# Kernel tuning notes

Hardware: AMD Instinct MI355X
Metric: run time of the kernel (lower is better)

## Reference

```python
import jax, jax.numpy as jnp
import numpy as np

PATCH_SIZE = 128
IMG = 256


def _circle_perimeter(r_o, c_o, radius):
    # skimage.draw.circle_perimeter, method='bresenham' (midpoint circle),
    # including the duplicate octant-boundary points that skimage emits.
    rr, cc = [], []
    c, r = 0, radius
    d = 3 - 2 * radius
    while c <= r:
        rr += [r, -r, r, -r, c, -c, c, -c]
        cc += [c, c, -c, -c, r, r, -r, -r]
        if d < 0:
            d += 4 * c + 6
        else:
            d += 4 * (c - r) + 10
            r -= 1
        c += 1
    return np.asarray(rr) + r_o, np.asarray(cc) + c_o


def _radial_indices(patch_size, img):
    cy, cx = img // 2, img // 2
    rr_all, cc_all, seg_all = [], [], []
    for radius in range(1, patch_size - 1):  # radii 1..patch_size-2
        rr, cc = _circle_perimeter(cy, cx, radius)
        rr_all.append(rr)
        cc_all.append(cc)
        seg_all.append(np.full(rr.shape[0], radius - 1))
    return (np.concatenate(rr_all).astype(np.int32),
            np.concatenate(cc_all).astype(np.int32),
            np.concatenate(seg_all).astype(np.int32))


def setup_inputs() -> dict:
    key = jax.random.key(0)
    k1, k2 = jax.random.split(key)
    inp = jax.random.normal(k1, (64, 3, IMG, IMG), dtype=jnp.float32)
    tgt = jax.random.normal(k2, (64, 3, IMG, IMG), dtype=jnp.float32)
    w = np.float32(np.arange(0, 1, 1 / (PATCH_SIZE - 1)))  # length 127
    weights = jnp.asarray(w / np.sum(w))
    rr_idx, cc_idx, seg_ids = _radial_indices(PATCH_SIZE, IMG)
    return {"input": inp, "target": tgt, "weights": weights,
            "rr_idx": jnp.asarray(rr_idx), "cc_idx": jnp.asarray(cc_idx),
            "seg_ids": jnp.asarray(seg_ids)}


def reference(input, target, weights, rr_idx, cc_idx, seg_ids):
    B, C = input.shape[0], input.shape[1]
    R = weights.shape[0]          # patch_size - 1 curve bins
    nseg = R - 1                  # radii 1..patch_size-2
    f1 = jnp.fft.fft2(input)      # complex64 [B,C,H,W]
    f2 = jnp.fft.fft2(target)
    p1 = f1[:, :, rr_idx, cc_idx]  # [B,C,Ntot]
    p2 = f2[:, :, rr_idx, cc_idx]
    # original sums num/den over ALL dims (batch+channel+perimeter points)
    cross = jnp.sum(p1 * jnp.conj(p2), axis=(0, 1))        # [Ntot] complex
    pw1 = jnp.sum(jnp.abs(p1) ** 2, axis=(0, 1))           # [Ntot]
    pw2 = jnp.sum(jnp.abs(p2) ** 2, axis=(0, 1))
    num = jnp.abs(jax.ops.segment_sum(cross, seg_ids, num_segments=nseg))
    den = (jax.ops.segment_sum(pw1, seg_ids, num_segments=nseg) *
           jax.ops.segment_sum(pw2, seg_ids, num_segments=nseg))
    curve = jnp.concatenate([jnp.ones((1,), jnp.float32),
                             (num / jnp.sqrt(den)).astype(jnp.float32)])  # [R]
    # curve is identical across (b, c); Linear(R,1,bias=False) then total sum
    curve_full = jnp.broadcast_to(curve, (B, C, R))
    return jnp.sum(curve_full @ weights)
```

## Files before the change

kernel.cpp:

```cpp
#include <hip/hip_runtime.h>
#include <math.h>

#define NSEG 126

__device__ __forceinline__ unsigned bitrev8(unsigned v) { return __brev(v) >> 24; }

template <int K>
__device__ __forceinline__ void fftK(float2 x[][4], int lane) {
    const float PI = 3.14159265358979323846f;
    {
        float s, c;
        __sincosf(-PI * (float)lane * (1.0f / 128.0f), &s, &c);
        #pragma unroll
        for (int k = 0; k < K; k++) {
            float2 u, t, d;
            u = x[k][0]; t = x[k][2];
            x[k][0] = make_float2(u.x + t.x, u.y + t.y);
            d = make_float2(u.x - t.x, u.y - t.y);
            x[k][2] = make_float2(d.x * c - d.y * s, d.x * s + d.y * c);
            u = x[k][1]; t = x[k][3];
            x[k][1] = make_float2(u.x + t.x, u.y + t.y);
            d = make_float2(u.x - t.x, u.y - t.y);
            x[k][3] = make_float2(d.x * s + d.y * c, -d.x * c + d.y * s);
        }
    }
    {
        float s, c;
        __sincosf(-PI * (float)lane * (1.0f / 64.0f), &s, &c);
        #pragma unroll
        for (int k = 0; k < K; k++) {
            float2 u, t, d;
            u = x[k][0]; t = x[k][1];
            x[k][0] = make_float2(u.x + t.x, u.y + t.y);
            d = make_float2(u.x - t.x, u.y - t.y);
            x[k][1] = make_float2(d.x * c - d.y * s, d.x * s + d.y * c);
            u = x[k][2]; t = x[k][3];
            x[k][2] = make_float2(u.x + t.x, u.y + t.y);
            d = make_float2(u.x - t.x, u.y - t.y);
            x[k][3] = make_float2(d.x * c - d.y * s, d.x * s + d.y * c);
        }
    }
    #pragma unroll
    for (int hbit = 5; hbit >= 0; hbit--) {
        int h = 1 << hbit;
        int j = lane & (h - 1);
        float s, c;
        __sincosf(-PI * (float)j / (float)h, &s, &c);
        bool up = (lane & h) != 0;
        #pragma unroll
        for (int k = 0; k < K; k++) {
            #pragma unroll
            for (int i = 0; i < 4; i++) {
                float px = __shfl_xor(x[k][i].x, h);
                float py = __shfl_xor(x[k][i].y, h);
                if (up) {
                    float dx = px - x[k][i].x, dy = py - x[k][i].y;
                    x[k][i] = make_float2(dx * c - dy * s, dx * s + dy * c);
                } else {
                    x[k][i] = make_float2(x[k][i].x + px, x[k][i].y + py);
                }
            }
        }
    }
}

__global__ void prep_zero(float* acc, int* counts) {
    int i = threadIdx.x;
    if (i < NSEG * 3) acc[i] = 0.f;
    if (i < 128) counts[i] = 0;
}

__device__ __forceinline__ bool keep_point(int r, int c) {
    return (c > 128) || (c == 128 && r > 128);
}

__global__ void prep_hist(const int* __restrict__ rr, const int* __restrict__ cc,
                          int n, int* counts) {
    int i = blockIdx.x * 256 + threadIdx.x;
    if (i < n) {
        int c = cc[i], r = rr[i];
        if (keep_point(r, c)) atomicAdd(&counts[255 - c], 1);
    }
}

__global__ void prep_scan(const int* __restrict__ counts, int* starts, int* cursor) {
    int lane = threadIdx.x;
    int2 c = reinterpret_cast<const int2*>(counts)[lane];
    int lsum = c.x + c.y;
    int pre = lsum;
    #pragma unroll
    for (int off = 1; off < 64; off <<= 1) {
        int v = __shfl_up(pre, off);
        if (lane >= off) pre += v;
    }
    int excl = pre - lsum;
    int2 outv = make_int2(excl, excl + c.x);
    reinterpret_cast<int2*>(starts)[lane] = outv;
    reinterpret_cast<int2*>(cursor)[lane] = outv;
    if (lane == 63) starts[128] = excl + c.x + c.y;
}

__global__ void prep_scatter(const int* __restrict__ rr, const int* __restrict__ cc,
                             const int* __restrict__ seg, int n, int* cursor,
                             int* b_pack) {
    int i = blockIdx.x * 256 + threadIdx.x;
    if (i < n) {
        int c = cc[i], r = rr[i];
        if (keep_point(r, c)) {
            int j = 255 - c;
            int pos = atomicAdd(&cursor[j], 1);
            int pr = (int)bitrev8((unsigned)r);
            int pm = (int)bitrev8((unsigned)(256 - r) & 255);
            b_pack[pos] = pr | (pm << 8) | (seg[i] << 16);
        }
    }
}

__global__ __launch_bounds__(512) void rowfft_kernel(
    const float* __restrict__ inp, const float* __restrict__ tgt,
    float2* __restrict__ G, int pair_base)
{
    __shared__ float2 T[256 * 17];
    int bid    = blockIdx.x;
    int plocal = bid >> 4;
    int rowgrp = bid & 15;
    int wv     = threadIdx.x >> 6;
    int lane   = threadIdx.x & 63;
    size_t base = (((size_t)(pair_base + plocal)) << 16)
                + ((size_t)((rowgrp << 4) + (wv << 1)) << 8);
    const float* s1 = inp + base;
    const float* s2 = tgt + base;

    float2 x[2][4];
    #pragma unroll
    for (int k = 0; k < 2; k++)
        #pragma unroll
        for (int i = 0; i < 4; i++) {
            int e = (k << 8) + i * 64 + lane;
            x[k][i] = make_float2(s1[e], s2[e]);
        }
    fftK<2>(x, lane);

    #pragma unroll
    for (int k = 0; k < 2; k++)
        #pragma unroll
        for (int i = 0; i < 4; i++)
            T[(i * 64 + lane) * 17 + (wv << 1) + k] = x[k][i];
    __syncthreads();

    float2* dst = G + (((size_t)plocal) << 16) + (rowgrp << 4);
    int xl = threadIdx.x & 15;
    int qb = threadIdx.x >> 4;
    #pragma unroll
    for (int ii = 0; ii < 8; ii++) {
        int q = qb + (ii << 5);
        dst[q * 256 + xl] = T[q * 17 + xl];
    }
}

__global__ __launch_bounds__(256) void colfft_gather_kernel(
    const float2* __restrict__ G, const int* __restrict__ starts,
    const int* __restrict__ b_pack, float* __restrict__ acc)
{
    __shared__ float2 Fb[4][2][256];
    __shared__ float accl[NSEG * 3];
    int tid    = threadIdx.x;
    int wv     = tid >> 6;
    int lane   = tid & 63;
    int plocal = blockIdx.x >> 4;
    int b      = blockIdx.x & 15;
    int jbase  = (b << 3) + (wv << 1);

    for (int i = tid; i < NSEG * 3; i += 256) accl[i] = 0.f;
    __syncthreads();

    const float2* Gp = G + (((size_t)plocal) << 16);
    int cols[4];
    cols[0] = jbase + 1;   cols[1] = 255 - jbase;
    cols[2] = jbase + 2;   cols[3] = 254 - jbase;

    float2 x[4][4];
    #pragma unroll
    for (int k = 0; k < 4; k++) {
        int q = (int)bitrev8((unsigned)cols[k]);
        const float2* col = Gp + ((size_t)q << 8);
        #pragma unroll
        for (int i = 0; i < 4; i++) x[k][i] = col[i * 64 + lane];
    }

    fftK<4>(x, lane);

    float2* F_lo = &Fb[wv][0][0];
    float2* F_hi = &Fb[wv][1][0];
    #pragma unroll
    for (int kb = 0; kb < 2; kb++) {
        #pragma unroll
        for (int i = 0; i < 4; i++) {
            F_lo[i * 64 + lane] = x[2 * kb + 0][i];
            F_hi[i * 64 + lane] = x[2 * kb + 1][i];
        }
        int j = jbase + kb;
        int s0 = starts[j], s1 = starts[j + 1];
        int e  = s0 + lane;
        int pk = (e < s1) ? b_pack[e] : 0;
        while (e < s1) {
            int e2  = e + 64;
            int pk2 = (e2 < s1) ? b_pack[e2] : 0;
            float2 a = F_hi[pk & 255];
            float2 m = F_lo[(pk >> 8) & 255];
            int sg = pk >> 16;
            float f1x = a.x + m.x, f1y = a.y - m.y;
            float dx  = a.x - m.x, dy  = a.y + m.y;
            atomicAdd(&accl[sg * 3 + 0], f1x * dy - f1y * dx);
            atomicAdd(&accl[sg * 3 + 1], f1x * f1x + f1y * f1y);
            atomicAdd(&accl[sg * 3 + 2], dx * dx + dy * dy);
            e = e2; pk = pk2;
        }
    }
    __syncthreads();

    for (int i = tid; i < NSEG * 3; i += 256) {
        float v = accl[i];
        if (v != 0.f) atomicAdd(&acc[i], v);
    }
}

__global__ void final_kernel(const float* __restrict__ acc, const float* __restrict__ w,
                             float* __restrict__ out, float scale) {
    int lane = threadIdx.x;
    float val = 0.f;
    for (int s = lane; s < NSEG; s += 64) {
        float cr = acc[s * 3 + 0];
        float p1 = acc[s * 3 + 1];
        float p2 = acc[s * 3 + 2];
        float den = p1 * p2;
        float curve = den > 0.f ? fabsf(cr) * rsqrtf(den) : 0.f;
        val += curve * w[s + 1];
    }
    if (lane == 0) val += w[0];
    #pragma unroll
    for (int off = 32; off > 0; off >>= 1) val += __shfl_down(val, off);
    if (lane == 0) out[0] = scale * val;
}

extern "C" void kernel_launch(void* const* d_in, const int* in_sizes, int n_in,
                              void* d_out, int out_size, void* d_ws, size_t ws_size,
                              hipStream_t stream)
{
    const float* inp = (const float*)d_in[0];
    const float* tgt = (const float*)d_in[1];
    const float* wts = (const float*)d_in[2];
    const int*   rr  = (const int*)d_in[3];
    const int*   cc  = (const int*)d_in[4];
    const int*   sg  = (const int*)d_in[5];
    int npts   = in_sizes[3];
    int npairs = in_sizes[0] >> 16;

    char* ws = (char*)d_ws;
    float* acc    = (float*)(ws + 0);
    int*   counts = (int*)(ws + 2048);
    int*   starts = (int*)(ws + 2560);
    int*   cursor = (int*)(ws + 3584);
    int*   b_pack = (int*)(ws + 4096);
    size_t goff = 4096 + (size_t)npts * 4;
    goff = (goff + 255) & ~(size_t)255;
    float2* G = (float2*)(ws + goff);

    size_t per_pair = (size_t)256 * 256 * sizeof(float2);
    int maxchunk = (int)((ws_size > goff ? (ws_size - goff) : 0) / per_pair);
    if (maxchunk < 1) maxchunk = 1;
    if (maxchunk > npairs) maxchunk = npairs;

    prep_zero<<<1, 512, 0, stream>>>(acc, counts);
    prep_hist<<<(npts + 255) / 256, 256, 0, stream>>>(rr, cc, npts, counts);
    prep_scan<<<1, 64, 0, stream>>>(counts, starts, cursor);
    prep_scatter<<<(npts + 255) / 256, 256, 0, stream>>>(rr, cc, sg, npts, cursor, b_pack);

    for (int pb = 0; pb < npairs; pb += maxchunk) {
        int cp = npairs - pb < maxchunk ? npairs - pb : maxchunk;
        rowfft_kernel<<<cp * 16, 512, 0, stream>>>(inp, tgt, G, pb);
        colfft_gather_kernel<<<cp * 16, 256, 0, stream>>>(G, starts, b_pack, acc);
    }

    final_kernel<<<1, 64, 0, stream>>>(acc, wts, (float*)d_out, (float)npairs);
}
```

Before: 267.5 us.

## Replace shuffle-based radix-2 FFT with register radix-16x16 FFT through LDS

```diff
diff --git a/kernel.cpp b/kernel.cpp
--- a/kernel.cpp
+++ b/kernel.cpp
@@ -2,66 +2,66 @@
 #include <math.h>
 
 #define NSEG 126
-
-__device__ __forceinline__ unsigned bitrev8(unsigned v) { return __brev(v) >> 24; }
-
-template <int K>
-__device__ __forceinline__ void fftK(float2 x[][4], int lane) {
-    const float PI = 3.14159265358979323846f;
-    {
+#define PI_F 3.14159265358979323846f
+#define C8 0.92387953251128675613f
+#define S8 0.38268343236508977173f
+#define R2C 0.70710678118654752440f
+
+__device__ __forceinline__ float2 cadd(float2 a, float2 b){ return make_float2(a.x+b.x, a.y+b.y); }
+__device__ __forceinline__ float2 csub(float2 a, float2 b){ return make_float2(a.x-b.x, a.y-b.y); }
+__device__ __forceinline__ float2 cmulf(float2 a, float c, float s){
+    return make_float2(fmaf(-a.y, s, a.x*c), fmaf(a.x, s, a.y*c));
+}
+__device__ __forceinline__ float2 mulmi(float2 a){ return make_float2(a.y, -a.x); }
+
+__device__ __forceinline__ void fft16(float2 a[16]) {
+    float2 u, d;
+    u=a[0]; d=csub(a[0],a[8]);  a[0]=cadd(u,a[8]);   a[8]=d;
+    u=a[1]; d=csub(a[1],a[9]);  a[1]=cadd(u,a[9]);   a[9]=cmulf(d,  C8, -S8);
+    u=a[2]; d=csub(a[2],a[10]); a[2]=cadd(u,a[10]);  a[10]=cmulf(d, R2C, -R2C);
+    u=a[3]; d=csub(a[3],a[11]); a[3]=cadd(u,a[11]);  a[11]=cmulf(d,  S8, -C8);
+    u=a[4]; d=csub(a[4],a[12]); a[4]=cadd(u,a[12]);  a[12]=mulmi(d);
+    u=a[5]; d=csub(a[5],a[13]); a[5]=cadd(u,a[13]);  a[13]=cmulf(d, -S8, -C8);
+    u=a[6]; d=csub(a[6],a[14]); a[6]=cadd(u,a[14]);  a[14]=cmulf(d, -R2C, -R2C);
+    u=a[7]; d=csub(a[7],a[15]); a[7]=cadd(u,a[15]);  a[15]=cmulf(d, -C8, -S8);
+    #pragma unroll
+    for (int h = 0; h < 16; h += 8) {
+        u=a[h+0]; d=csub(a[h+0],a[h+4]); a[h+0]=cadd(u,a[h+4]); a[h+4]=d;
+        u=a[h+1]; d=csub(a[h+1],a[h+5]); a[h+1]=cadd(u,a[h+5]); a[h+5]=cmulf(d, R2C, -R2C);
+        u=a[h+2]; d=csub(a[h+2],a[h+6]); a[h+2]=cadd(u,a[h+6]); a[h+6]=mulmi(d);
+        u=a[h+3]; d=csub(a[h+3],a[h+7]); a[h+3]=cadd(u,a[h+7]); a[h+7]=cmulf(d, -R2C, -R2C);
+    }
+    #pragma unroll
+    for (int q = 0; q < 16; q += 4) {
+        u=a[q+0]; d=csub(a[q+0],a[q+2]); a[q+0]=cadd(u,a[q+2]); a[q+2]=d;
+        u=a[q+1]; d=csub(a[q+1],a[q+3]); a[q+1]=cadd(u,a[q+3]); a[q+3]=mulmi(d);
+    }
+    #pragma unroll
+    for (int p = 0; p < 16; p += 2) {
+        u=a[p]; a[p]=cadd(u,a[p+1]); a[p+1]=csub(u,a[p+1]);
+    }
+}
+
+__device__ __constant__ int BR4[16] = {0,8,4,12,2,10,6,14,1,9,5,13,3,11,7,15};
+
+__device__ __forceinline__ void fft256_core(float2 x[16], float2* gb, int r) {
+    fft16(x);
+    #pragma unroll
+    for (int m = 1; m < 16; m++) {
         float s, c;
-        __sincosf(-PI * (float)lane * (1.0f / 128.0f), &s, &c);
-        #pragma unroll
-        for (int k = 0; k < K; k++) {
-            float2 u, t, d;
-            u = x[k][0]; t = x[k][2];
-            x[k][0] = make_float2(u.x + t.x, u.y + t.y);
-            d = make_float2(u.x - t.x, u.y - t.y);
-            x[k][2] = make_float2(d.x * c - d.y * s, d.x * s + d.y * c);
-            u = x[k][1]; t = x[k][3];
-            x[k][1] = make_float2(u.x + t.x, u.y + t.y);
-            d = make_float2(u.x - t.x, u.y - t.y);
-            x[k][3] = make_float2(d.x * s + d.y * c, -d.x * c + d.y * s);
-        }
-    }
-    {
-        float s, c;
-        __sincosf(-PI * (float)lane * (1.0f / 64.0f), &s, &c);
-        #pragma unroll
-        for (int k = 0; k < K; k++) {
-            float2 u, t, d;
-            u = x[k][0]; t = x[k][1];
-            x[k][0] = make_float2(u.x + t.x, u.y + t.y);
-            d = make_float2(u.x - t.x, u.y - t.y);
-            x[k][1] = make_float2(d.x * c - d.y * s, d.x * s + d.y * c);
-            u = x[k][2]; t = x[k][3];
-            x[k][2] = make_float2(u.x + t.x, u.y + t.y);
-            d = make_float2(u.x - t.x, u.y - t.y);
-            x[k][3] = make_float2(d.x * c - d.y * s, d.x * s + d.y * c);
-        }
-    }
-    #pragma unroll
-    for (int hbit = 5; hbit >= 0; hbit--) {
-        int h = 1 << hbit;
-        int j = lane & (h - 1);
-        float s, c;
-        __sincosf(-PI * (float)j / (float)h, &s, &c);
-        bool up = (lane & h) != 0;
-        #pragma unroll
-        for (int k = 0; k < K; k++) {
-            #pragma unroll
-            for (int i = 0; i < 4; i++) {
-                float px = __shfl_xor(x[k][i].x, h);
-                float py = __shfl_xor(x[k][i].y, h);
-                if (up) {
-                    float dx = px - x[k][i].x, dy = py - x[k][i].y;
-                    x[k][i] = make_float2(dx * c - dy * s, dx * s + dy * c);
-                } else {
-                    x[k][i] = make_float2(x[k][i].x + px, x[k][i].y + py);
-                }
-            }
-        }
-    }
+        __sincosf(-(PI_F / 128.0f) * (float)(r * BR4[m]), &s, &c);
+        x[m] = cmulf(x[m], c, s);
+    }
+    #pragma unroll
+    for (int m = 0; m < 16; m++)
+        gb[BR4[m] * 16 + ((r + BR4[m]) & 15)] = x[m];
+    float2 z[16];
+    #pragma unroll
+    for (int n1 = 0; n1 < 16; n1++)
+        z[n1] = gb[r * 16 + ((n1 + r) & 15)];
+    fft16(z);
+    #pragma unroll
+    for (int m = 0; m < 16; m++) x[m] = z[m];
 }
 
 __global__ void prep_zero(float* acc, int* counts) {
@@ -109,97 +109,107 @@
         if (keep_point(r, c)) {
             int j = 255 - c;
             int pos = atomicAdd(&cursor[j], 1);
-            int pr = (int)bitrev8((unsigned)r);
-            int pm = (int)bitrev8((unsigned)(256 - r) & 255);
-            b_pack[pos] = pr | (pm << 8) | (seg[i] << 16);
+            b_pack[pos] = r | (((256 - r) & 255) << 8) | (seg[i] << 16);
         }
     }
 }
 
-__global__ __launch_bounds__(512) void rowfft_kernel(
+__global__ __launch_bounds__(128, 4) void rowfft_kernel(
     const float* __restrict__ inp, const float* __restrict__ tgt,
     float2* __restrict__ G, int pair_base)
 {
-    __shared__ float2 T[256 * 17];
+    __shared__ float2 lds[256 * 9];
+    int tid    = threadIdx.x;
+    int wv     = tid >> 6;
+    int lane   = tid & 63;
+    int g      = lane >> 4;
+    int r      = lane & 15;
     int bid    = blockIdx.x;
-    int plocal = bid >> 4;
-    int rowgrp = bid & 15;
-    int wv     = threadIdx.x >> 6;
-    int lane   = threadIdx.x & 63;
-    size_t base = (((size_t)(pair_base + plocal)) << 16)
-                + ((size_t)((rowgrp << 4) + (wv << 1)) << 8);
-    const float* s1 = inp + base;
-    const float* s2 = tgt + base;
-
-    float2 x[2][4];
-    #pragma unroll
-    for (int k = 0; k < 2; k++)
-        #pragma unroll
-        for (int i = 0; i < 4; i++) {
-            int e = (k << 8) + i * 64 + lane;
-            x[k][i] = make_float2(s1[e], s2[e]);
-        }
-    fftK<2>(x, lane);
-
-    #pragma unroll
-    for (int k = 0; k < 2; k++)
-        #pragma unroll
-        for (int i = 0; i < 4; i++)
-            T[(i * 64 + lane) * 17 + (wv << 1) + k] = x[k][i];
-    __syncthreads();
-
-    float2* dst = G + (((size_t)plocal) << 16) + (rowgrp << 4);
-    int xl = threadIdx.x & 15;
-    int qb = threadIdx.x >> 4;
-    #pragma unroll
-    for (int ii = 0; ii < 8; ii++) {
-        int q = qb + (ii << 5);
-        dst[q * 256 + xl] = T[q * 17 + xl];
-    }
-}
-
-__global__ __launch_bounds__(256) void colfft_gather_kernel(
+    int plocal = bid >> 5;
+    int rowgrp = bid & 31;
+    int row    = (rowgrp << 3) + (wv << 2) + g;
+    size_t base = (((size_t)(pair_base + plocal)) << 16) + ((size_t)row << 8) + (r << 4);
+    const float4* s1 = (const float4*)(inp + base);
+    const float4* s2 = (const float4*)(tgt + base);
+
+    float4 A[4], B[4];
+    #pragma unroll
+    for (int i = 0; i < 4; i++) { A[i] = s1[i]; B[i] = s2[i]; }
+    float2 x[16];
+    #pragma unroll
+    for (int i = 0; i < 4; i++) {
+        x[4*i+0] = make_float2(A[i].x, B[i].x);
+        x[4*i+1] = make_float2(A[i].y, B[i].y);
+        x[4*i+2] = make_float2(A[i].z, B[i].z);
+        x[4*i+3] = make_float2(A[i].w, B[i].w);
+    }
+    float2* gb = lds + wv * 1040 + g * 260;
+    #pragma unroll
+    for (int n1 = 0; n1 < 16; n1++)
+        gb[n1 * 16 + ((r + n1) & 15)] = x[n1];
+    float2 y[16];
+    #pragma unroll
+    for (int n2 = 0; n2 < 16; n2++)
+        y[n2] = gb[r * 16 + ((n2 + r) & 15)];
+
+    fft256_core(y, gb, r);
+
+    __syncthreads();
+    int lrow = (wv << 2) + g;
+    #pragma unroll
+    for (int m = 0; m < 16; m++)
+        lds[(r + 16 * BR4[m]) * 9 + lrow] = y[m];
+    __syncthreads();
+
+    float2* dst = G + (((size_t)plocal) << 16) + (rowgrp << 3);
+    int xl = tid & 7;
+    int q8 = tid >> 3;
+    #pragma unroll
+    for (int ii = 0; ii < 16; ii++) {
+        int q = q8 + (ii << 4);
+        dst[q * 256 + xl] = lds[q * 9 + xl];
+    }
+}
+
+__global__ __launch_bounds__(128, 4) void colfft_gather_kernel(
     const float2* __restrict__ G, const int* __restrict__ starts,
     const int* __restrict__ b_pack, float* __restrict__ acc)
 {
-    __shared__ float2 Fb[4][2][256];
+    __shared__ float2 wbufs[2 * 1040];
     __shared__ float accl[NSEG * 3];
     int tid    = threadIdx.x;
     int wv     = tid >> 6;
     int lane   = tid & 63;
-    int plocal = blockIdx.x >> 4;
-    int b      = blockIdx.x & 15;
-    int jbase  = (b << 3) + (wv << 1);
-
-    for (int i = tid; i < NSEG * 3; i += 256) accl[i] = 0.f;
-    __syncthreads();
-
-    const float2* Gp = G + (((size_t)plocal) << 16);
-    int cols[4];
-    cols[0] = jbase + 1;   cols[1] = 255 - jbase;
-    cols[2] = jbase + 2;   cols[3] = 254 - jbase;
-
-    float2 x[4][4];
-    #pragma unroll
-    for (int k = 0; k < 4; k++) {
-        int q = (int)bitrev8((unsigned)cols[k]);
-        const float2* col = Gp + ((size_t)q << 8);
-        #pragma unroll
-        for (int i = 0; i < 4; i++) x[k][i] = col[i * 64 + lane];
-    }
-
-    fftK<4>(x, lane);
-
-    float2* F_lo = &Fb[wv][0][0];
-    float2* F_hi = &Fb[wv][1][0];
+    int g      = lane >> 4;
+    int r      = lane & 15;
+    int plocal = blockIdx.x >> 5;
+    int b      = blockIdx.x & 31;
+    int jbase  = (b << 2) + (wv << 1);
+
+    for (int i = tid; i < NSEG * 3; i += 128) accl[i] = 0.f;
+    __syncthreads();
+
+    int c = (g == 0) ? (jbase + 1) : (g == 1) ? (255 - jbase)
+          : (g == 2) ? (jbase + 2) : (254 - jbase);
+    const float2* col = G + (((size_t)plocal) << 16) + ((size_t)c << 8) + r;
+
+    float2 x[16];
+    #pragma unroll
+    for (int n2 = 0; n2 < 16; n2++) x[n2] = col[n2 << 4];
+
+    float2* gb = wbufs + wv * 1040 + g * 260;
+    fft256_core(x, gb, r);
+
+    #pragma unroll
+    for (int m = 0; m < 16; m++)
+        gb[r + 16 * BR4[m]] = x[m];
+
+    float2* wbuf = wbufs + wv * 1040;
     #pragma unroll
     for (int kb = 0; kb < 2; kb++) {
-        #pragma unroll
-        for (int i = 0; i < 4; i++) {
-            F_lo[i * 64 + lane] = x[2 * kb + 0][i];
-            F_hi[i * 64 + lane] = x[2 * kb + 1][i];
-        }
         int j = jbase + kb;
+        const float2* F_lo = wbuf + (2 * kb) * 260;
+        const float2* F_hi = wbuf + (2 * kb + 1) * 260;
         int s0 = starts[j], s1 = starts[j + 1];
         int e  = s0 + lane;
         int pk = (e < s1) ? b_pack[e] : 0;
@@ -219,7 +229,7 @@
     }
     __syncthreads();
 
-    for (int i = tid; i < NSEG * 3; i += 256) {
+    for (int i = tid; i < NSEG * 3; i += 128) {
         float v = accl[i];
         if (v != 0.f) atomicAdd(&acc[i], v);
     }
@@ -278,8 +288,8 @@
 
     for (int pb = 0; pb < npairs; pb += maxchunk) {
         int cp = npairs - pb < maxchunk ? npairs - pb : maxchunk;
-        rowfft_kernel<<<cp * 16, 512, 0, stream>>>(inp, tgt, G, pb);
-        colfft_gather_kernel<<<cp * 16, 256, 0, stream>>>(G, starts, b_pack, acc);
+        rowfft_kernel<<<cp * 32, 128, 0, stream>>>(inp, tgt, G, pb);
+        colfft_gather_kernel<<<cp * 32, 128, 0, stream>>>(G, starts, b_pack, acc);
     }
 
     final_kernel<<<1, 64, 0, stream>>>(acc, wts, (float*)d_out, (float)npairs);
```

Result: slower. 312.7 us (+16.9%).

## Store row FFT output row-major and transpose via shared tile in column pass

Applied to the files above, without the earlier changes.

```diff
diff --git a/kernel.cpp b/kernel.cpp
--- a/kernel.cpp
+++ b/kernel.cpp
@@ -64,10 +64,9 @@
     }
 }
 
-__global__ void prep_zero(float* acc, int* counts) {
+__global__ void prep_zero(int* counts) {
     int i = threadIdx.x;
-    if (i < NSEG * 3) acc[i] = 0.f;
-    if (i < 128) counts[i] = 0;
+    counts[i] = 0;
 }
 
 __device__ __forceinline__ bool keep_point(int r, int c) {
@@ -116,98 +115,105 @@
     }
 }
 
-__global__ __launch_bounds__(512) void rowfft_kernel(
+__global__ __launch_bounds__(512, 2) void rowfft_kernel(
     const float* __restrict__ inp, const float* __restrict__ tgt,
     float2* __restrict__ G, int pair_base)
 {
-    __shared__ float2 T[256 * 17];
-    int bid    = blockIdx.x;
-    int plocal = bid >> 4;
-    int rowgrp = bid & 15;
-    int wv     = threadIdx.x >> 6;
-    int lane   = threadIdx.x & 63;
-    size_t base = (((size_t)(pair_base + plocal)) << 16)
-                + ((size_t)((rowgrp << 4) + (wv << 1)) << 8);
-    const float* s1 = inp + base;
-    const float* s2 = tgt + base;
-
-    float2 x[2][4];
-    #pragma unroll
-    for (int k = 0; k < 2; k++)
+    int tid    = threadIdx.x;
+    int wv     = tid >> 6;
+    int lane   = tid & 63;
+    int plocal = blockIdx.x >> 3;
+    int rowgrp = blockIdx.x & 7;
+    int row0   = (rowgrp << 5) + (wv << 2);
+    int b6     = (int)(__brev((unsigned)lane) >> 26);
+
+    size_t ibase = (((size_t)(pair_base + plocal)) << 16) + ((size_t)row0 << 8);
+    const float* s1 = inp + ibase;
+    const float* s2 = tgt + ibase;
+
+    float2 x[4][4];
+    #pragma unroll
+    for (int k = 0; k < 4; k++)
         #pragma unroll
         for (int i = 0; i < 4; i++) {
-            int e = (k << 8) + i * 64 + lane;
+            int e = (k << 8) + (i << 6) + lane;
             x[k][i] = make_float2(s1[e], s2[e]);
         }
-    fftK<2>(x, lane);
-
-    #pragma unroll
-    for (int k = 0; k < 2; k++)
-        #pragma unroll
-        for (int i = 0; i < 4; i++)
-            T[(i * 64 + lane) * 17 + (wv << 1) + k] = x[k][i];
-    __syncthreads();
-
-    float2* dst = G + (((size_t)plocal) << 16) + (rowgrp << 4);
-    int xl = threadIdx.x & 15;
-    int qb = threadIdx.x >> 4;
-    #pragma unroll
-    for (int ii = 0; ii < 8; ii++) {
-        int q = qb + (ii << 5);
-        dst[q * 256 + xl] = T[q * 17 + xl];
-    }
-}
-
-__global__ __launch_bounds__(256) void colfft_gather_kernel(
+
+    fftK<4>(x, lane);
+
+    float2* dst = G + (((size_t)plocal) << 16) + ((size_t)row0 << 8) + (b6 << 2);
+    #pragma unroll
+    for (int k = 0; k < 4; k++) {
+        float4* d4 = reinterpret_cast<float4*>(dst + (k << 8));
+        d4[0] = make_float4(x[k][0].x, x[k][0].y, x[k][2].x, x[k][2].y);
+        d4[1] = make_float4(x[k][1].x, x[k][1].y, x[k][3].x, x[k][3].y);
+    }
+}
+
+__global__ __launch_bounds__(512, 2) void colfft_gather_kernel(
     const float2* __restrict__ G, const int* __restrict__ starts,
-    const int* __restrict__ b_pack, float* __restrict__ acc)
+    const int* __restrict__ b_pack, float* __restrict__ partials, int row_base)
 {
-    __shared__ float2 Fb[4][2][256];
+    __shared__ float2 tile[256 * 33];
     __shared__ float accl[NSEG * 3];
     int tid    = threadIdx.x;
     int wv     = tid >> 6;
     int lane   = tid & 63;
-    int plocal = blockIdx.x >> 4;
-    int b      = blockIdx.x & 15;
-    int jbase  = (b << 3) + (wv << 1);
-
-    for (int i = tid; i < NSEG * 3; i += 256) accl[i] = 0.f;
+    int plocal = blockIdx.x >> 3;
+    int bq     = blockIdx.x & 7;
+    int jb     = bq << 4;
+
+    for (int i = tid; i < NSEG * 3; i += 512) accl[i] = 0.f;
+
+    const float2* Gp = G + (((size_t)plocal) << 16);
+    int lo_c = jb + 1, hi_c = 240 - jb;
+
+    #pragma unroll
+    for (int k = 0; k < 8; k++) {
+        int idx = tid + (k << 9);
+        int c16 = idx & 15, xx = idx >> 4;
+        tile[xx * 33 + c16] = Gp[xx * 256 + lo_c + c16];
+    }
+    #pragma unroll
+    for (int k = 0; k < 8; k++) {
+        int idx = tid + (k << 9);
+        int c16 = idx & 15, xx = idx >> 4;
+        tile[xx * 33 + 16 + c16] = Gp[xx * 256 + hi_c + c16];
+    }
     __syncthreads();
 
-    const float2* Gp = G + (((size_t)plocal) << 16);
-    int cols[4];
-    cols[0] = jbase + 1;   cols[1] = 255 - jbase;
-    cols[2] = jbase + 2;   cols[3] = 254 - jbase;
+    int colk[4];
+    colk[0] = 2 * wv;      colk[1] = 31 - 2 * wv;
+    colk[2] = 2 * wv + 1;  colk[3] = 30 - 2 * wv;
 
     float2 x[4][4];
     #pragma unroll
-    for (int k = 0; k < 4; k++) {
-        int q = (int)bitrev8((unsigned)cols[k]);
-        const float2* col = Gp + ((size_t)q << 8);
-        #pragma unroll
-        for (int i = 0; i < 4; i++) x[k][i] = col[i * 64 + lane];
-    }
+    for (int k = 0; k < 4; k++)
+        #pragma unroll
+        for (int i = 0; i < 4; i++)
+            x[k][i] = tile[((i << 6) + lane) * 33 + colk[k]];
+    __syncthreads();
 
     fftK<4>(x, lane);
 
-    float2* F_lo = &Fb[wv][0][0];
-    float2* F_hi = &Fb[wv][1][0];
+    float2* slot = tile + (wv << 9);
     #pragma unroll
     for (int kb = 0; kb < 2; kb++) {
         #pragma unroll
         for (int i = 0; i < 4; i++) {
-            F_lo[i * 64 + lane] = x[2 * kb + 0][i];
-            F_hi[i * 64 + lane] = x[2 * kb + 1][i];
-        }
-        int j = jbase + kb;
+            slot[(i << 6) + lane]       = x[2 * kb + 0][i];
+            slot[256 + (i << 6) + lane] = x[2 * kb + 1][i];
+        }
+        int j = jb + 2 * wv + kb;
         int s0 = starts[j], s1 = starts[j + 1];
         int e  = s0 + lane;
         int pk = (e < s1) ? b_pack[e] : 0;
         while (e < s1) {
             int e2  = e + 64;
             int pk2 = (e2 < s1) ? b_pack[e2] : 0;
-            float2 a = F_hi[pk & 255];
-            float2 m = F_lo[(pk >> 8) & 255];
+            float2 a = slot[256 + (pk & 255)];
+            float2 m = slot[(pk >> 8) & 255];
             int sg = pk >> 16;
             float f1x = a.x + m.x, f1y = a.y - m.y;
             float dx  = a.x - m.x, dy  = a.y + m.y;
@@ -219,10 +225,24 @@
     }
     __syncthreads();
 
-    for (int i = tid; i < NSEG * 3; i += 256) {
-        float v = accl[i];
-        if (v != 0.f) atomicAdd(&acc[i], v);
-    }
+    float* prow = partials + (size_t)(row_base + blockIdx.x) * 384;
+    for (int i = tid; i < NSEG * 3; i += 512) prow[i] = accl[i];
+}
+
+__global__ void reduce_partials(const float* __restrict__ partials, int nrows,
+                                float* __restrict__ acc) {
+    int e = blockIdx.x * 64 + threadIdx.x;
+    if (e >= NSEG * 3) return;
+    float s0 = 0.f, s1 = 0.f, s2 = 0.f, s3 = 0.f;
+    int r = 0;
+    for (; r + 4 <= nrows; r += 4) {
+        s0 += partials[(size_t)(r + 0) * 384 + e];
+        s1 += partials[(size_t)(r + 1) * 384 + e];
+        s2 += partials[(size_t)(r + 2) * 384 + e];
+        s3 += partials[(size_t)(r + 3) * 384 + e];
+    }
+    for (; r < nrows; r++) s0 += partials[(size_t)r * 384 + e];
+    acc[e] = (s0 + s1) + (s2 + s3);
 }
 
 __global__ void final_kernel(const float* __restrict__ acc, const float* __restrict__ w,
@@ -262,7 +282,10 @@
     int*   starts = (int*)(ws + 2560);
     int*   cursor = (int*)(ws + 3584);
     int*   b_pack = (int*)(ws + 4096);
-    size_t goff = 4096 + (size_t)npts * 4;
+    size_t poff = 4096 + (size_t)npts * 4;
+    poff = (poff + 255) & ~(size_t)255;
+    float* partials = (float*)(ws + poff);
+    size_t goff = poff + (size_t)npairs * 8 * 384 * 4;
     goff = (goff + 255) & ~(size_t)255;
     float2* G = (float2*)(ws + goff);
 
@@ -271,16 +294,18 @@
     if (maxchunk < 1) maxchunk = 1;
     if (maxchunk > npairs) maxchunk = npairs;
 
-    prep_zero<<<1, 512, 0, stream>>>(acc, counts);
+    prep_zero<<<1, 128, 0, stream>>>(counts);
     prep_hist<<<(npts + 255) / 256, 256, 0, stream>>>(rr, cc, npts, counts);
     prep_scan<<<1, 64, 0, stream>>>(counts, starts, cursor);
     prep_scatter<<<(npts + 255) / 256, 256, 0, stream>>>(rr, cc, sg, npts, cursor, b_pack);
 
     for (int pb = 0; pb < npairs; pb += maxchunk) {
         int cp = npairs - pb < maxchunk ? npairs - pb : maxchunk;
-        rowfft_kernel<<<cp * 16, 512, 0, stream>>>(inp, tgt, G, pb);
-        colfft_gather_kernel<<<cp * 16, 256, 0, stream>>>(G, starts, b_pack, acc);
-    }
-
+        rowfft_kernel<<<cp * 8, 512, 0, stream>>>(inp, tgt, G, pb);
+        colfft_gather_kernel<<<cp * 8, 512, 0, stream>>>(G, starts, b_pack,
+                                                         partials, pb * 8);
+    }
+
+    reduce_partials<<<6, 64, 0, stream>>>(partials, npairs * 8, acc);
     final_kernel<<<1, 64, 0, stream>>>(acc, wts, (float*)d_out, (float)npairs);
 }
```

After: 387.9 us. 1.45x slower.
